# Kernel optimization log

Hardware: AMD Instinct MI355X
Metric: run time of the kernel (lower is better)

## Reference

```python
import jax, jax.numpy as jnp
import numpy as np

BRIGHTNESS_THRESHOLD = 0.4
NUM_BINS = 16


def _soft_histogram(x, mask):
    # x: [B, C, H, W], mask: [B, 1, H, W] (float 0/1)
    B, C, H, W = x.shape
    bin_centers = jnp.linspace(0.0, 1.0, NUM_BINS, dtype=x.dtype)  # [nb]
    bin_width = 1.0 / NUM_BINS
    inv_two_sigma2 = 1.0 / (2.0 * bin_width * bin_width)
    x_flat = x.reshape(B, C, H * W, 1)            # [B,C,HW,1]
    mask_flat = mask.reshape(B, 1, H * W, 1)      # [B,1,HW,1]
    weights = jnp.exp(-((x_flat - bin_centers) ** 2) * inv_two_sigma2)  # [B,C,HW,nb]
    hist = jnp.sum(weights * mask_flat, axis=2)   # [B,C,nb]
    hist = hist / (jnp.sum(hist, axis=-1, keepdims=True) + 1e-7)
    return hist


def setup_inputs() -> dict:
    key = jax.random.key(0)
    k1, k2 = jax.random.split(key)
    pred = jax.random.uniform(k1, (8, 3, 512, 512), dtype=jnp.float32)
    target = jax.random.uniform(k2, (8, 3, 512, 512), dtype=jnp.float32)
    return {"pred": pred, "target": target}


def reference(pred, target):
    target_brightness = jnp.mean(target, axis=1, keepdims=True)       # [B,1,H,W]
    bright_mask = (target_brightness > BRIGHTNESS_THRESHOLD).astype(pred.dtype)
    pred_hist = _soft_histogram(pred, bright_mask)
    target_hist = _soft_histogram(target, bright_mask)
    return jnp.mean(jnp.abs(pred_hist - target_hist))
```

## Files before the change

### kernel.cpp

```cpp
#include <hip/hip_runtime.h>

#define NB 16
#define BATCH 8
#define PLANE (512*512)
#define FBINS 1024
#define CHUNKS 128
#define THREADS 256
#define PX_PER_BLOCK (PLANE / CHUNKS)
#define GROUPS (PX_PER_BLOCK / (THREADS * 4))

#if __has_builtin(__builtin_amdgcn_exp2f)
__device__ __forceinline__ float exp2_fast(float x) { return __builtin_amdgcn_exp2f(x); }
#else
__device__ __forceinline__ float exp2_fast(float x) { return __expf(x * 0.69314718056f); }
#endif

#define NEG_C2 (-0.8207331788f)

__device__ __forceinline__ int qbin(float x) {
    int f = (int)(x * (float)FBINS);
    return f > (FBINS - 1) ? (FBINS - 1) : f;
}

__global__ __launch_bounds__(THREADS)
void count_kernel(const float* __restrict__ pred,
                  const float* __restrict__ tgt,
                  unsigned int* __restrict__ partial
                  )
{
    const int chunk = blockIdx.x;
    const int b     = blockIdx.y;
    const int tid   = threadIdx.x;

    __shared__ unsigned int cnt[3 * FBINS];
    #pragma unroll
    for (int k = 0; k < 3 * FBINS / THREADS; ++k)
        cnt[tid + k * THREADS] = 0u;
    __syncthreads();

    const float* pb = pred + (size_t)b * 3 * PLANE;
    const float* tb = tgt  + (size_t)b * 3 * PLANE;
    const int base = chunk * PX_PER_BLOCK + tid * 4;

    #pragma unroll
    for (int g = 0; g < GROUPS; ++g) {
        const int p = base + g * (THREADS * 4);
        const float4 P0 = *(const float4*)(pb + p);
        const float4 P1 = *(const float4*)(pb + PLANE + p);
        const float4 P2 = *(const float4*)(pb + 2 * PLANE + p);
        const float4 T0 = *(const float4*)(tb + p);
        const float4 T1 = *(const float4*)(tb + PLANE + p);
        const float4 T2 = *(const float4*)(tb + 2 * PLANE + p);

        const float p0a[4] = {P0.x, P0.y, P0.z, P0.w};
        const float p1a[4] = {P1.x, P1.y, P1.z, P1.w};
        const float p2a[4] = {P2.x, P2.y, P2.z, P2.w};
        const float t0a[4] = {T0.x, T0.y, T0.z, T0.w};
        const float t1a[4] = {T1.x, T1.y, T1.z, T1.w};
        const float t2a[4] = {T2.x, T2.y, T2.z, T2.w};

        #pragma unroll
        for (int j = 0; j < 4; ++j) {
            const bool m = (t0a[j] + t1a[j] + t2a[j]) * (1.0f / 3.0f) > 0.4f;
            if (m) {
                atomicAdd(&cnt[           qbin(p0a[j])], 1u);
                atomicAdd(&cnt[           qbin(p1a[j])], 65536u);
                atomicAdd(&cnt[FBINS    + qbin(p2a[j])], 1u);
                atomicAdd(&cnt[FBINS    + qbin(t0a[j])], 65536u);
                atomicAdd(&cnt[2*FBINS  + qbin(t1a[j])], 1u);
                atomicAdd(&cnt[2*FBINS  + qbin(t2a[j])], 65536u);
            }
        }
    }
    __syncthreads();

    #pragma unroll
    for (int k = 0; k < 3 * FBINS / THREADS; ++k) {
        const int w  = tid + k * THREADS;
        const int h2 = w >> 10;
        const int f  = w & (FBINS - 1);
        partial[(((size_t)h2 * BATCH + b) * CHUNKS + chunk) * FBINS + f] = cnt[w];
    }
}

__global__ __launch_bounds__(THREADS)
void combine_kernel(const unsigned int* __restrict__ partial,
                    float* __restrict__ hist)
{
    const int hb  = blockIdx.x;
    const int h   = hb / BATCH;
    const int b   = hb % BATCH;
    const int h2  = h >> 1;
    const int sh  = (h & 1) * 16;
    const int tid = threadIdx.x;

    unsigned int s[4] = {0u, 0u, 0u, 0u};
    const unsigned int* base =
        partial + (((size_t)h2 * BATCH + b) * CHUNKS) * FBINS + tid * 4;
    for (int c = 0; c < CHUNKS; ++c) {
        const uint4 v = *(const uint4*)(base + (size_t)c * FBINS);
        s[0] += (v.x >> sh) & 0xFFFFu;
        s[1] += (v.y >> sh) & 0xFFFFu;
        s[2] += (v.z >> sh) & 0xFFFFu;
        s[3] += (v.w >> sh) & 0xFFFFu;
    }

    float acc[NB];
    #pragma unroll
    for (int i = 0; i < NB; ++i) acc[i] = 0.0f;

    #pragma unroll
    for (int j = 0; j < 4; ++j) {
        const float cf = (float)s[j];
        const float y  = ((float)(tid * 4 + j) + 0.5f) * (15.0f / (float)FBINS);
        #pragma unroll
        for (int i = 0; i < NB; ++i) {
            const float u = y - (float)i;
            acc[i] = fmaf(cf, exp2_fast(u * u * NEG_C2), acc[i]);
        }
    }

    __shared__ float red[4][NB];
    const int lane = tid & 63;
    const int wv   = tid >> 6;
    #pragma unroll
    for (int i = 0; i < NB; ++i) {
        float v = acc[i];
        #pragma unroll
        for (int off = 32; off > 0; off >>= 1)
            v += __shfl_down(v, off, 64);
        if (lane == 0) red[wv][i] = v;
    }
    __syncthreads();
    if (tid < NB)
        hist[(size_t)hb * NB + tid] =
            red[0][tid] + red[1][tid] + red[2][tid] + red[3][tid];
}

__global__ void finalize_kernel(const float* __restrict__ hist,
                                float* __restrict__ out)
{
    const int t = threadIdx.x;
    const int b   = t / 48;
    const int rem = t % 48;
    const int c   = rem / NB;
    const int i   = rem % NB;

    const float* hp = hist + ((size_t)(c    ) * BATCH + b) * NB;
    const float* ht = hist + ((size_t)(c + 3) * BATCH + b) * NB;
    float sp = 0.0f, st = 0.0f;
    #pragma unroll
    for (int k = 0; k < NB; ++k) { sp += hp[k]; st += ht[k]; }

    float val = fabsf(hp[i] / (sp + 1e-7f) - ht[i] / (st + 1e-7f));

    #pragma unroll
    for (int off = 32; off > 0; off >>= 1)
        val += __shfl_down(val, off, 64);

    __shared__ float r[6];
    const int lane = t & 63, wv = t >> 6;
    if (lane == 0) r[wv] = val;
    __syncthreads();
    if (t == 0)
        out[0] = (r[0] + r[1] + r[2] + r[3] + r[4] + r[5]) * (1.0f / 384.0f);
}

extern "C" void kernel_launch(void* const* d_in, const int* in_sizes, int n_in,
                              void* d_out, int out_size, void* d_ws, size_t ws_size,
                              hipStream_t stream)
{
    const float* pred = (const float*)d_in[0];
    const float* tgt  = (const float*)d_in[1];

    unsigned int* partial = (unsigned int*)d_ws;
    float* hist = (float*)((char*)d_ws + (size_t)3 * BATCH * CHUNKS * FBINS * 4);

    count_kernel<<<dim3(CHUNKS, BATCH), THREADS, 0, stream>>>(pred, tgt, partial);
    combine_kernel<<<6 * BATCH, THREADS, 0, stream>>>(partial, hist);
    finalize_kernel<<<1, 384, 0, stream>>>(hist, (float*)d_out);
}
```

Measured before the change: 100.2 us.

## Halve fine bins and split combine across bin slices for more parallelism

Reduces the quantized fine-bin count from 1024 to 512, which halves the partial-count traffic written by the count kernel and read by the combine kernel. The combine kernel now launches 8 slices per histogram (384 blocks instead of 48), with each wave summing a quarter of the chunks. Per-slice results are written to a new buffer and summed in the finalize kernel. Coarser quantization adds approximation error to the soft-histogram weights, and the combine step now does extra shuffle reductions.

```diff
diff --git a/kernel.cpp b/kernel.cpp
--- a/kernel.cpp
+++ b/kernel.cpp
@@ -3,11 +3,13 @@
 #define NB 16
 #define BATCH 8
 #define PLANE (512*512)
-#define FBINS 1024
+#define FBINS 512
 #define CHUNKS 128
 #define THREADS 256
 #define PX_PER_BLOCK (PLANE / CHUNKS)
 #define GROUPS (PX_PER_BLOCK / (THREADS * 4))
+#define SLICES 8
+#define FPB (FBINS / SLICES)
 
 #if __has_builtin(__builtin_amdgcn_exp2f)
 __device__ __forceinline__ float exp2_fast(float x) { return __builtin_amdgcn_exp2f(x); }
@@ -77,7 +79,7 @@
     #pragma unroll
     for (int k = 0; k < 3 * FBINS / THREADS; ++k) {
         const int w  = tid + k * THREADS;
-        const int h2 = w >> 10;
+        const int h2 = w >> 9;
         const int f  = w & (FBINS - 1);
         partial[(((size_t)h2 * BATCH + b) * CHUNKS + chunk) * FBINS + f] = cnt[w];
     }
@@ -85,69 +87,77 @@
 
 __global__ __launch_bounds__(THREADS)
 void combine_kernel(const unsigned int* __restrict__ partial,
-                    float* __restrict__ hist)
+                    float* __restrict__ out2 )
 {
-    const int hb  = blockIdx.x;
-    const int h   = hb / BATCH;
-    const int b   = hb % BATCH;
-    const int h2  = h >> 1;
-    const int sh  = (h & 1) * 16;
-    const int tid = threadIdx.x;
+    const int slice = blockIdx.x;
+    const int hb    = blockIdx.y;
+    const int h     = hb / BATCH;
+    const int b     = hb % BATCH;
+    const int h2    = h >> 1;
+    const int sh    = (h & 1) * 16;
+    const int tid   = threadIdx.x;
 
-    unsigned int s[4] = {0u, 0u, 0u, 0u};
+    const int f_loc = tid & (FPB - 1);
+    const int q     = tid >> 6;
+    const int f     = slice * FPB + f_loc;
+
     const unsigned int* base =
-        partial + (((size_t)h2 * BATCH + b) * CHUNKS) * FBINS + tid * 4;
-    for (int c = 0; c < CHUNKS; ++c) {
-        const uint4 v = *(const uint4*)(base + (size_t)c * FBINS);
-        s[0] += (v.x >> sh) & 0xFFFFu;
-        s[1] += (v.y >> sh) & 0xFFFFu;
-        s[2] += (v.z >> sh) & 0xFFFFu;
-        s[3] += (v.w >> sh) & 0xFFFFu;
-    }
+        partial + (((size_t)h2 * BATCH + b) * CHUNKS + q * 32) * FBINS + f;
+    unsigned int s = 0u;
+    #pragma unroll 8
+    for (int c = 0; c < 32; ++c)
+        s += (base[(size_t)c * FBINS] >> sh) & 0xFFFFu;
 
-    float acc[NB];
-    #pragma unroll
-    for (int i = 0; i < NB; ++i) acc[i] = 0.0f;
+    __shared__ unsigned int red[4][FPB];
+    red[q][f_loc] = s;
+    __syncthreads();
 
-    #pragma unroll
-    for (int j = 0; j < 4; ++j) {
-        const float cf = (float)s[j];
-        const float y  = ((float)(tid * 4 + j) + 0.5f) * (15.0f / (float)FBINS);
+    if (tid < FPB) {
+        const float cf = (float)(red[0][tid] + red[1][tid] + red[2][tid] + red[3][tid]);
+        const float y  = ((float)(slice * FPB + tid) + 0.5f) * (15.0f / (float)FBINS);
+
+        float acc[NB];
         #pragma unroll
         for (int i = 0; i < NB; ++i) {
             const float u = y - (float)i;
-            acc[i] = fmaf(cf, exp2_fast(u * u * NEG_C2), acc[i]);
+            acc[i] = cf * exp2_fast(u * u * NEG_C2);
+        }
+        #pragma unroll
+        for (int off = 32; off > 0; off >>= 1)
+            #pragma unroll
+            for (int i = 0; i < NB; ++i)
+                acc[i] += __shfl_down(acc[i], off, 64);
+
+        if (tid == 0) {
+            float* o = out2 + ((size_t)slice * 48 + hb) * NB;
+            #pragma unroll
+            for (int i = 0; i < NB; ++i) o[i] = acc[i];
         }
     }
-
-    __shared__ float red[4][NB];
-    const int lane = tid & 63;
-    const int wv   = tid >> 6;
-    #pragma unroll
-    for (int i = 0; i < NB; ++i) {
-        float v = acc[i];
-        #pragma unroll
-        for (int off = 32; off > 0; off >>= 1)
-            v += __shfl_down(v, off, 64);
-        if (lane == 0) red[wv][i] = v;
-    }
-    __syncthreads();
-    if (tid < NB)
-        hist[(size_t)hb * NB + tid] =
-            red[0][tid] + red[1][tid] + red[2][tid] + red[3][tid];
 }
 
-__global__ void finalize_kernel(const float* __restrict__ hist,
+__global__ void finalize_kernel(const float* __restrict__ out2,
                                 float* __restrict__ out)
 {
     const int t = threadIdx.x;
+    __shared__ float H[48 * NB];
+
+    for (int e = t; e < 48 * NB; e += 384) {
+        float v = 0.0f;
+        #pragma unroll
+        for (int s = 0; s < SLICES; ++s)
+            v += out2[(size_t)s * 48 * NB + e];
+        H[e] = v;
+    }
+    __syncthreads();
+
     const int b   = t / 48;
     const int rem = t % 48;
     const int c   = rem / NB;
     const int i   = rem % NB;
 
-    const float* hp = hist + ((size_t)(c    ) * BATCH + b) * NB;
-    const float* ht = hist + ((size_t)(c + 3) * BATCH + b) * NB;
+    const float* hp = H + ((c    ) * BATCH + b) * NB;
+    const float* ht = H + ((c + 3) * BATCH + b) * NB;
     float sp = 0.0f, st = 0.0f;
     #pragma unroll
     for (int k = 0; k < NB; ++k) { sp += hp[k]; st += ht[k]; }
@@ -174,9 +184,9 @@
     const float* tgt  = (const float*)d_in[1];
 
     unsigned int* partial = (unsigned int*)d_ws;
-    float* hist = (float*)((char*)d_ws + (size_t)3 * BATCH * CHUNKS * FBINS * 4);
+    float* out2 = (float*)((char*)d_ws + (size_t)3 * BATCH * CHUNKS * FBINS * 4);
 
     count_kernel<<<dim3(CHUNKS, BATCH), THREADS, 0, stream>>>(pred, tgt, partial);
-    combine_kernel<<<6 * BATCH, THREADS, 0, stream>>>(partial, hist);
-    finalize_kernel<<<1, 384, 0, stream>>>(hist, (float*)d_out);
+    combine_kernel<<<dim3(SLICES, 48), THREADS, 0, stream>>>(partial, out2);
+    finalize_kernel<<<1, 384, 0, stream>>>(out2, (float*)d_out);
 }
```

After: 90.89 us. -9.3%, faster.
